# Kernel optimization log

Hardware: AMD Instinct MI355X
Metric: run time of the kernel (lower is better)

## Reference

```python
import jax, jax.numpy as jnp
import numpy as np

N, D, B = 50000, 256, 2048
SIGMA = 1.0
SIGMA2 = SIGMA * SIGMA  # module stores np.square(sigma)


def setup_inputs() -> dict:
    key = jax.random.key(0)
    k1, k2, k3, k4 = jax.random.split(key, 4)
    x = jax.random.normal(k1, (B, D), dtype=jnp.float32)
    data_set = jax.random.normal(k2, (N, D), dtype=jnp.float32)
    # labels are +/-1
    data_labels = jnp.where(jax.random.uniform(k3, (N,)) < 0.5, -1.0, 1.0).astype(jnp.float32)
    # lambdas initialized to ones in the module; use small positive noise around 1/n scale
    lambdas = jax.random.uniform(k4, (N,), dtype=jnp.float32) * (2.0 / N)
    b = jnp.ones((1,), dtype=jnp.float32)
    return {"x": x, "data_set": data_set, "data_labels": data_labels,
            "lambdas": lambdas, "b": b}


def reference(x, data_set, data_labels, lambdas, b):
    x2 = jnp.sum(x * x, axis=1, keepdims=True)            # [B,1]
    s2 = jnp.sum(data_set * data_set, axis=1)             # [N]
    cross = jnp.einsum('bd,nd->bn', x, data_set)          # [B,N]
    sqdist = x2 + s2[None, :] - 2.0 * cross               # [B,N]
    K = jnp.exp(-sqdist / (2.0 * SIGMA2))                 # rbf kernel [B,N]
    w = data_labels * jax.nn.relu(lambdas)                # [N]
    return jnp.tanh(K @ w + b)                            # [B]
```

## Files before the change

### kernel.cpp

```cpp
#include <hip/hip_runtime.h>
#include <hip/hip_bf16.h>
#include <math.h>

#define NPTS 50000
#define DIM  256
#define BQ   2048
#define NPAD 50048

#define BK   32
#define CH   64
#define NCH  782
#define NG   48
#define LOG2E 1.4426950408889634f

#define WS_ACC 0
#define WS_X2  2048
#define WS_T   4096
#define WS_SGN 54144
#define WS_XB  104192
#define WS_SB  366336
#define WS_TOTAL_BYTES (6772480ull * 4ull)

#define V1_ACC 0
#define V1_X2  2048
#define V1_S2  4096
#define V1_W   54096

typedef __bf16 bf16x8 __attribute__((ext_vector_type(8)));
typedef __bf16 bf16x4 __attribute__((ext_vector_type(4)));
typedef float  f32x4  __attribute__((ext_vector_type(4)));
typedef unsigned int u32;

__device__ __forceinline__ float fast_exp2(float v) {
#if __has_builtin(__builtin_amdgcn_exp2f)
  return __builtin_amdgcn_exp2f(v);
#else
  return exp2f(v);
#endif
}

__device__ __forceinline__ void async_copy16(const __bf16* g, __bf16* l) {
  __builtin_amdgcn_global_load_lds(
      (const __attribute__((address_space(1))) u32*)g,
      (__attribute__((address_space(3))) u32*)l, 16, 0, 0);
}


__global__ __launch_bounds__(256) void svm_precvt9(
    const float* __restrict__ x, const float* __restrict__ s,
    const float* __restrict__ labels, const float* __restrict__ lambdas,
    float* __restrict__ ws) {
  const int wid  = blockIdx.x * 4 + (threadIdx.x >> 6);
  const int lane = threadIdx.x & 63;
  __bf16* xb = (__bf16*)(ws + WS_XB);
  __bf16* sb = (__bf16*)(ws + WS_SB);

  if (blockIdx.x < 8) ws[WS_ACC + blockIdx.x * 256 + threadIdx.x] = 0.0f;

  if (wid < NPAD) {
    float4 v = make_float4(0.f, 0.f, 0.f, 0.f);
    if (wid < NPTS)
      v = reinterpret_cast<const float4*>(s + (size_t)wid * DIM)[lane];
    bf16x4 h = { (__bf16)v.x, (__bf16)v.y, (__bf16)v.z, (__bf16)v.w };
    *reinterpret_cast<bf16x4*>(sb + (size_t)wid * DIM + lane * 4) = h;
    float ss = v.x * v.x + v.y * v.y + v.z * v.z + v.w * v.w;
    #pragma unroll
    for (int off = 32; off > 0; off >>= 1) ss += __shfl_xor(ss, off);
    if (lane == 0) {
      float s2h = 0.5f * LOG2E * ss;
      float lam = (wid < NPTS) ? lambdas[wid] : 0.0f;
      float lab = (wid < NPTS) ? labels[wid] : 1.0f;
      float mag = lam > 0.0f ? lam : 0.0f;
      ws[WS_T + wid]   = (mag > 0.0f) ? s2h - log2f(mag) : __builtin_inff();
      ws[WS_SGN + wid] = lab;
    }
  } else if (wid < NPAD + BQ) {
    int r = wid - NPAD;
    float4 v = reinterpret_cast<const float4*>(x + (size_t)r * DIM)[lane];
    bf16x4 h = { (__bf16)v.x, (__bf16)v.y, (__bf16)v.z, (__bf16)v.w };
    *reinterpret_cast<bf16x4*>(xb + (size_t)r * DIM + lane * 4) = h;
    float ss = v.x * v.x + v.y * v.y + v.z * v.z + v.w * v.w;
    #pragma unroll
    for (int off = 32; off > 0; off >>= 1) ss += __shfl_xor(ss, off);
    if (lane == 0) ws[WS_X2 + r] = 0.5f * LOG2E * ss;
  }
}

__global__ __launch_bounds__(256, 2) void svm_main9(float* __restrict__ ws) {
  __shared__ __bf16 sB[8 * CH * 32];

  const __bf16* xb = (const __bf16*)(ws + WS_XB);
  const __bf16* sb = (const __bf16*)(ws + WS_SB);
  const float* x2g = ws + WS_X2;
  const float* tg  = ws + WS_T;
  const float* sgg = ws + WS_SGN;
  float* accOut    = ws + WS_ACC;

  const int t    = threadIdx.x;
  const int wave = t >> 6;
  const int lane = t & 63;
  const int quad = lane >> 4;
  const int l16  = lane & 15;
  const int g    = blockIdx.x & 47;
  const int mt   = blockIdx.x / 48;
  const int m0   = mt * 128;
  const int c0   = (NCH * g) / NG;
  const int c1   = (NCH * (g + 1)) / NG;

  f32x4 afr[2][8];
  #pragma unroll
  for (int mi = 0; mi < 2; ++mi)
    #pragma unroll
    for (int kt = 0; kt < 8; ++kt)
      afr[mi][kt] = *reinterpret_cast<const f32x4*>(
          xb + (size_t)(m0 + wave * 32 + mi * 16 + l16) * DIM + kt * BK + quad * 8);
  #pragma unroll
  for (int mi = 0; mi < 2; ++mi)
    #pragma unroll
    for (int kt = 0; kt < 8; ++kt)
      asm volatile("" : "+v"(afr[mi][kt]));

  float runAcc[2][4] = {{0.f, 0.f, 0.f, 0.f}, {0.f, 0.f, 0.f, 0.f}};

  const int srcswz = ((lane & 3) ^ ((lane >> 3) & 3)) * 8;
  const int rdswz = (quad ^ ((l16 >> 1) & 3)) * 8;

  for (int c = c0; c < c1; ++c) {
    __syncthreads();

    #pragma unroll
    for (int i = 0; i < 8; ++i) {
      int ch = wave * 8 + i;
      int kt = ch >> 2;
      int nb = (ch & 3) * 16;
      const __bf16* src = sb + (size_t)(c * CH + nb + (lane >> 2)) * DIM
                             + kt * BK + srcswz;
      async_copy16(src, &sB[kt * (CH * 32) + nb * 32] + lane * 8);
    }
    __syncthreads();

    f32x4 acc[2][4];
    #pragma unroll
    for (int mi = 0; mi < 2; ++mi)
      #pragma unroll
      for (int ni = 0; ni < 4; ++ni)
        acc[mi][ni] = (f32x4)(0.0f);

    #pragma unroll
    for (int kt = 0; kt < 8; ++kt) {
      bf16x8 bfv[4];
      #pragma unroll
      for (int ni = 0; ni < 4; ++ni)
        bfv[ni] = *reinterpret_cast<const bf16x8*>(
            &sB[kt * (CH * 32) + (ni * 16 + l16) * 32 + rdswz]);
      #pragma unroll
      for (int mi = 0; mi < 2; ++mi)
        #pragma unroll
        for (int ni = 0; ni < 4; ++ni)
          acc[mi][ni] = __builtin_amdgcn_mfma_f32_16x16x32_bf16(
              __builtin_bit_cast(bf16x8, afr[mi][kt]), bfv[ni],
              acc[mi][ni], 0, 0, 0);
    }

    float tt[4], sg[4];
    #pragma unroll
    for (int ni = 0; ni < 4; ++ni) {
      int n = c * CH + ni * 16 + l16;
      tt[ni] = tg[n];
      sg[ni] = sgg[n];
    }
    #pragma unroll
    for (int mi = 0; mi < 2; ++mi)
      #pragma unroll
      for (int reg = 0; reg < 4; ++reg) {
        float p = runAcc[mi][reg];
        #pragma unroll
        for (int ni = 0; ni < 4; ++ni)
          p = __builtin_fmaf(sg[ni],
                fast_exp2(__builtin_fmaf(acc[mi][ni][reg], LOG2E, -tt[ni])), p);
        runAcc[mi][reg] = p;
      }
  }

  #pragma unroll
  for (int mi = 0; mi < 2; ++mi)
    #pragma unroll
    for (int reg = 0; reg < 4; ++reg) {
      float v = runAcc[mi][reg];
      v += __shfl_xor(v, 1);
      v += __shfl_xor(v, 2);
      v += __shfl_xor(v, 4);
      v += __shfl_xor(v, 8);
      if (l16 == 0) {
        int row = m0 + wave * 32 + mi * 16 + quad * 4 + reg;
        atomicAdd(&accOut[row], fast_exp2(-x2g[row]) * v);
      }
    }
}


__global__ __launch_bounds__(256) void svm_precompute(
    const float* __restrict__ x, const float* __restrict__ s,
    const float* __restrict__ labels, const float* __restrict__ lambdas,
    float* __restrict__ ws) {
  int wid  = blockIdx.x * 4 + (threadIdx.x >> 6);
  int lane = threadIdx.x & 63;
  const float* src;
  if (wid < NPTS)           src = s + (size_t)wid * DIM;
  else if (wid < NPTS + BQ) src = x + (size_t)(wid - NPTS) * DIM;
  else return;
  float4 v = reinterpret_cast<const float4*>(src)[lane];
  float ss = v.x * v.x + v.y * v.y + v.z * v.z + v.w * v.w;
  #pragma unroll
  for (int off = 32; off > 0; off >>= 1) ss += __shfl_xor(ss, off);
  if (lane == 0) {
    if (wid < NPTS) {
      ws[V1_S2 + wid] = ss;
      float lam = lambdas[wid];
      ws[V1_W + wid] = labels[wid] * (lam > 0.0f ? lam : 0.0f);
    } else {
      ws[V1_X2 + (wid - NPTS)] = ss;
    }
  }
}

__global__ __launch_bounds__(256) void svm_main(
    const float* __restrict__ x, const float* __restrict__ s,
    const float* __restrict__ ws) {
  __shared__ __bf16 sA[128 * BK];
  __shared__ __bf16 sB2[128 * BK];

  const int t    = threadIdx.x;
  const int wave = t >> 6;
  const int lane = t & 63;
  const int quad = lane >> 4;
  const int l16  = lane & 15;
  const int wm   = (wave & 1) * 64;
  const int wn   = (wave >> 1) * 64;
  const int bRow0 = blockIdx.y * 128;
  const int n0    = blockIdx.x * 128;

  f32x4 acc[4][4];
  #pragma unroll
  for (int i = 0; i < 4; ++i)
    #pragma unroll
    for (int j = 0; j < 4; ++j)
      acc[i][j] = (f32x4)(0.0f);

  for (int kt = 0; kt < DIM / BK; ++kt) {
    const int k0 = kt * BK;
    __syncthreads();
    #pragma unroll
    for (int i = 0; i < 4; ++i) {
      int slot = t + i * 256;
      int r  = slot >> 3;
      int c4 = slot & 7;
      float4 va = reinterpret_cast<const float4*>(
          x + (size_t)(bRow0 + r) * DIM + k0)[c4];
      bf16x4 ha = { (__bf16)va.x, (__bf16)va.y, (__bf16)va.z, (__bf16)va.w };
      *reinterpret_cast<bf16x4*>(&sA[r * BK + c4 * 4]) = ha;

      int nrow = n0 + r;
      float4 vb = make_float4(0.f, 0.f, 0.f, 0.f);
      if (nrow < NPTS)
        vb = reinterpret_cast<const float4*>(
            s + (size_t)nrow * DIM + k0)[c4];
      bf16x4 hb = { (__bf16)vb.x, (__bf16)vb.y, (__bf16)vb.z, (__bf16)vb.w };
      *reinterpret_cast<bf16x4*>(&sB2[r * BK + c4 * 4]) = hb;
    }
    __syncthreads();

    bf16x8 af[4], bfv[4];
    #pragma unroll
    for (int mi = 0; mi < 4; ++mi)
      af[mi] = *reinterpret_cast<const bf16x8*>(
          &sA[(wm + mi * 16 + l16) * BK + quad * 8]);
    #pragma unroll
    for (int ni = 0; ni < 4; ++ni)
      bfv[ni] = *reinterpret_cast<const bf16x8*>(
          &sB2[(wn + ni * 16 + l16) * BK + quad * 8]);
    #pragma unroll
    for (int mi = 0; mi < 4; ++mi)
      #pragma unroll
      for (int ni = 0; ni < 4; ++ni)
        acc[mi][ni] = __builtin_amdgcn_mfma_f32_16x16x32_bf16(
            af[mi], bfv[ni], acc[mi][ni], 0, 0, 0);
  }

  const float* x2g = ws + V1_X2;
  const float* s2g = ws + V1_S2;
  const float* wg  = ws + V1_W;
  float* accOut    = (float*)ws + V1_ACC;

  float s2v[4], wv[4];
  #pragma unroll
  for (int ni = 0; ni < 4; ++ni) {
    int n = n0 + wn + ni * 16 + l16;
    bool ok = n < NPTS;
    s2v[ni] = ok ? s2g[n] : 0.0f;
    wv[ni]  = ok ? wg[n]  : 0.0f;
  }
  #pragma unroll
  for (int mi = 0; mi < 4; ++mi) {
    const int mbase = wm + mi * 16 + quad * 4;
    #pragma unroll
    for (int reg = 0; reg < 4; ++reg) {
      float x2r = x2g[bRow0 + mbase + reg];
      float ps = 0.0f;
      #pragma unroll
      for (int ni = 0; ni < 4; ++ni) {
        float cc = acc[mi][ni][reg];
        ps += __expf(__builtin_fmaf(-0.5f, x2r + s2v[ni], cc)) * wv[ni];
      }
      ps += __shfl_xor(ps, 1);
      ps += __shfl_xor(ps, 2);
      ps += __shfl_xor(ps, 4);
      ps += __shfl_xor(ps, 8);
      if (l16 == 0) atomicAdd(&accOut[bRow0 + mbase + reg], ps);
    }
  }
}


__global__ __launch_bounds__(256) void svm_finalize(
    const float* __restrict__ ws, const float* __restrict__ bias,
    float* __restrict__ out) {
  int i = blockIdx.x * 256 + threadIdx.x;
  if (i < BQ) out[i] = tanhf(ws[i] + bias[0]);
}

extern "C" void kernel_launch(void* const* d_in, const int* in_sizes, int n_in,
                              void* d_out, int out_size, void* d_ws, size_t ws_size,
                              hipStream_t stream) {
  const float* x       = (const float*)d_in[0];
  const float* s       = (const float*)d_in[1];
  const float* labels  = (const float*)d_in[2];
  const float* lambdas = (const float*)d_in[3];
  const float* bias    = (const float*)d_in[4];
  float* out = (float*)d_out;
  float* ws  = (float*)d_ws;

  if (ws_size >= WS_TOTAL_BYTES) {
    svm_precvt9<<<(NPAD + BQ + 3) / 4, 256, 0, stream>>>(x, s, labels, lambdas, ws);
    svm_main9<<<16 * NG, 256, 0, stream>>>(ws);
  } else {
    hipMemsetAsync(ws, 0, BQ * sizeof(float), stream);
    svm_precompute<<<(NPTS + BQ + 3) / 4, 256, 0, stream>>>(x, s, labels, lambdas, ws);
    dim3 grid(391, BQ / 128);
    svm_main<<<grid, 256, 0, stream>>>(x, s, ws);
  }
  svm_finalize<<<BQ / 256, 256, 0, stream>>>(ws, bias, out);
}
```

Before: 156.9 us.

## Double-buffer LDS staging and enlarge per-block query tile to 256 rows

Adds a second LDS buffer so the async copy of the next support-vector chunk is issued before the MFMA and exp work on the current chunk. One barrier per iteration replaces two. Each block now handles 256 query rows (4 fragments per wave) instead of 128, so every staged chunk is reused across twice as many rows. The N dimension is split into 64 groups, giving 512 blocks instead of 768. In exchange, register pressure from 128 VGPRs of A fragments plus 64 of accumulators rises, and the kernel uses twice the LDS.

After: 179.2 us. 1.14x slower.

```diff
diff --git a/kernel.cpp b/kernel.cpp
--- a/kernel.cpp
+++ b/kernel.cpp
@@ -10,7 +10,7 @@
 #define BK   32
 #define CH   64
 #define NCH  782
-#define NG   48
+#define NG   64
 #define LOG2E 1.4426950408889634f
 
 #define WS_ACC 0
@@ -86,8 +86,8 @@
   }
 }
 
-__global__ __launch_bounds__(256, 2) void svm_main9(float* __restrict__ ws) {
-  __shared__ __bf16 sB[8 * CH * 32];
+__global__ __launch_bounds__(256, 2) void svm_main10(float* __restrict__ ws) {
+  __shared__ __bf16 sB[2][8 * CH * 32];
 
   const __bf16* xb = (const __bf16*)(ws + WS_XB);
   const __bf16* sb = (const __bf16*)(ws + WS_SB);
@@ -101,47 +101,63 @@
   const int lane = t & 63;
   const int quad = lane >> 4;
   const int l16  = lane & 15;
-  const int g    = blockIdx.x & 47;
-  const int mt   = blockIdx.x / 48;
-  const int m0   = mt * 128;
+  const int g    = blockIdx.x & (NG - 1);
+  const int mt   = blockIdx.x / NG;
+  const int m0   = mt * 256;
   const int c0   = (NCH * g) / NG;
   const int c1   = (NCH * (g + 1)) / NG;
 
-  f32x4 afr[2][8];
-  #pragma unroll
-  for (int mi = 0; mi < 2; ++mi)
+  const int srcswz = ((lane & 3) ^ ((lane >> 3) & 3)) * 8;
+  const int rdswz = (quad ^ ((l16 >> 1) & 3)) * 8;
+
+#define STAGE10(buf, cc)                                                      \
+  do {                                                                        \
+    _Pragma("unroll")                                                         \
+    for (int i = 0; i < 8; ++i) {                                             \
+      int chn = wave * 8 + i;                                      \
+      int kt = chn >> 2;                                           \
+      int nb = (chn & 3) * 16;                                \
+      const __bf16* src = sb + (size_t)((cc) * CH + nb + (lane >> 2)) * DIM   \
+                             + kt * BK + srcswz;                              \
+      async_copy16(src, &sB[(buf)][kt * (CH * 32) + nb * 32] + lane * 8);     \
+    }                                                                         \
+  } while (0)
+
+  STAGE10(0, c0);
+
+  f32x4 afr[4][8];
+  #pragma unroll
+  for (int mi = 0; mi < 4; ++mi)
     #pragma unroll
     for (int kt = 0; kt < 8; ++kt)
       afr[mi][kt] = *reinterpret_cast<const f32x4*>(
-          xb + (size_t)(m0 + wave * 32 + mi * 16 + l16) * DIM + kt * BK + quad * 8);
-  #pragma unroll
-  for (int mi = 0; mi < 2; ++mi)
+          xb + (size_t)(m0 + wave * 64 + mi * 16 + l16) * DIM + kt * BK + quad * 8);
+  #pragma unroll
+  for (int mi = 0; mi < 4; ++mi)
     #pragma unroll
     for (int kt = 0; kt < 8; ++kt)
       asm volatile("" : "+v"(afr[mi][kt]));
 
-  float runAcc[2][4] = {{0.f, 0.f, 0.f, 0.f}, {0.f, 0.f, 0.f, 0.f}};
-
-  const int srcswz = ((lane & 3) ^ ((lane >> 3) & 3)) * 8;
-  const int rdswz = (quad ^ ((l16 >> 1) & 3)) * 8;
-
+  float runAcc[4][4] = {{0.f, 0.f, 0.f, 0.f}, {0.f, 0.f, 0.f, 0.f},
+                        {0.f, 0.f, 0.f, 0.f}, {0.f, 0.f, 0.f, 0.f}};
+
+  __syncthreads();
+
+  int cur = 0;
   for (int c = c0; c < c1; ++c) {
-    __syncthreads();
-
-    #pragma unroll
-    for (int i = 0; i < 8; ++i) {
-      int ch = wave * 8 + i;
-      int kt = ch >> 2;
-      int nb = (ch & 3) * 16;
-      const __bf16* src = sb + (size_t)(c * CH + nb + (lane >> 2)) * DIM
-                             + kt * BK + srcswz;
-      async_copy16(src, &sB[kt * (CH * 32) + nb * 32] + lane * 8);
-    }
-    __syncthreads();
-
-    f32x4 acc[2][4];
-    #pragma unroll
-    for (int mi = 0; mi < 2; ++mi)
+    if (c + 1 < c1) STAGE10(cur ^ 1, c + 1);
+
+    float tt[4], sg[4];
+    #pragma unroll
+    for (int ni = 0; ni < 4; ++ni) {
+      int n = c * CH + ni * 16 + l16;
+      tt[ni] = tg[n];
+      sg[ni] = sgg[n];
+    }
+
+    f32x4 acc[4][4];
+    #pragma unroll
+    for (int mi = 0; mi < 4; ++mi)
       #pragma unroll
       for (int ni = 0; ni < 4; ++ni)
         acc[mi][ni] = (f32x4)(0.0f);
@@ -152,9 +168,9 @@
       #pragma unroll
       for (int ni = 0; ni < 4; ++ni)
         bfv[ni] = *reinterpret_cast<const bf16x8*>(
-            &sB[kt * (CH * 32) + (ni * 16 + l16) * 32 + rdswz]);
-      #pragma unroll
-      for (int mi = 0; mi < 2; ++mi)
+            &sB[cur][kt * (CH * 32) + (ni * 16 + l16) * 32 + rdswz]);
+      #pragma unroll
+      for (int mi = 0; mi < 4; ++mi)
         #pragma unroll
         for (int ni = 0; ni < 4; ++ni)
           acc[mi][ni] = __builtin_amdgcn_mfma_f32_16x16x32_bf16(
@@ -162,15 +178,8 @@
               acc[mi][ni], 0, 0, 0);
     }
 
-    float tt[4], sg[4];
-    #pragma unroll
-    for (int ni = 0; ni < 4; ++ni) {
-      int n = c * CH + ni * 16 + l16;
-      tt[ni] = tg[n];
-      sg[ni] = sgg[n];
-    }
-    #pragma unroll
-    for (int mi = 0; mi < 2; ++mi)
+    #pragma unroll
+    for (int mi = 0; mi < 4; ++mi)
       #pragma unroll
       for (int reg = 0; reg < 4; ++reg) {
         float p = runAcc[mi][reg];
@@ -180,10 +189,13 @@
                 fast_exp2(__builtin_fmaf(acc[mi][ni][reg], LOG2E, -tt[ni])), p);
         runAcc[mi][reg] = p;
       }
-  }
-
-  #pragma unroll
-  for (int mi = 0; mi < 2; ++mi)
+
+    __syncthreads();
+    cur ^= 1;
+  }
+
+  #pragma unroll
+  for (int mi = 0; mi < 4; ++mi)
     #pragma unroll
     for (int reg = 0; reg < 4; ++reg) {
       float v = runAcc[mi][reg];
@@ -192,10 +204,11 @@
       v += __shfl_xor(v, 4);
       v += __shfl_xor(v, 8);
       if (l16 == 0) {
-        int row = m0 + wave * 32 + mi * 16 + quad * 4 + reg;
+        int row = m0 + wave * 64 + mi * 16 + quad * 4 + reg;
         atomicAdd(&accOut[row], fast_exp2(-x2g[row]) * v);
       }
     }
+#undef STAGE10
 }
 
 
@@ -342,7 +355,7 @@
 
   if (ws_size >= WS_TOTAL_BYTES) {
     svm_precvt9<<<(NPAD + BQ + 3) / 4, 256, 0, stream>>>(x, s, labels, lambdas, ws);
-    svm_main9<<<16 * NG, 256, 0, stream>>>(ws);
+    svm_main10<<<8 * NG, 256, 0, stream>>>(ws);
   } else {
     hipMemsetAsync(ws, 0, BQ * sizeof(float), stream);
     svm_precompute<<<(NPTS + BQ + 3) / 4, 256, 0, stream>>>(x, s, labels, lambdas, ws);
```
